# Performance work log

Hardware: AMD Instinct MI355X
Metric: run time of the kernel (lower is better)

Reference implementation:

```python
import jax, jax.numpy as jnp
import numpy as np

B, R, DIM = 4096, 64, 128


def setup_inputs() -> dict:
    key = jax.random.key(0)
    ks = jax.random.split(key, 8)
    return {
        "query_emb": jax.random.normal(ks[0], (B, DIM), jnp.float32),
        "offset_emb": jax.random.normal(ks[1], (B, DIM), jnp.float32),
        "refer_embs": jax.random.normal(ks[2], (B, R, DIM), jnp.float32),
        "query_r": jax.random.normal(ks[3], (B, DIM), jnp.float32),
        "refer_r": jax.random.normal(ks[4], (B, R, DIM), jnp.float32),
        "start_embs": jax.random.normal(ks[5], (B, R, DIM), jnp.float32),
        # attn_layer_1: Linear(2*dim, dim); xavier-uniform-like scale
        "W1": jax.random.uniform(ks[6], (DIM, 2 * DIM), jnp.float32, -0.125, 0.125),
        "b1": jnp.zeros((DIM,), jnp.float32),
        # attn_layer_2: Linear(dim, dim)
        "W2": jax.random.uniform(ks[7], (DIM, DIM), jnp.float32, -0.125, 0.125),
        "b2": jnp.zeros((DIM,), jnp.float32),
    }


def reference(query_emb, offset_emb, refer_embs, query_r, refer_r, start_embs, W1, b1, W2, b2):
    # bias term per neighbor: [B, R, dim]
    bias = refer_embs - (start_embs + refer_r)
    # concat([refer_r, broadcast(query_r)]) @ W1.T split to avoid materializing the concat:
    # W1 = [W1_a | W1_b] over the 2*dim input axis
    W1a, W1b = W1[:, :DIM], W1[:, DIM:]
    h = jnp.einsum('brd,kd->brk', refer_r, W1a) \
        + jnp.einsum('bd,kd->bk', query_r, W1b)[:, None, :] + b1
    h = jax.nn.relu(h)  # [B, R, dim]
    attn = jnp.einsum('brk,dk->brd', h, W2) + b2  # attn_layer_2
    final_refer_emb = jnp.sum(attn * bias, axis=-2)  # [B, dim]
    final_query_emb = query_emb + final_refer_emb
    return (final_query_emb, offset_emb)
```

## Files before the change

### kernel.cpp

```cpp
#include <hip/hip_runtime.h>
#include <hip/hip_bf16.h>
#include <stdint.h>

#define BTOT 4096
#define RR   64
#define DIMD 128
#define NB   8
#define NBLK (BTOT / NB)

typedef short s16x8 __attribute__((ext_vector_type(8)));
typedef float f32x4 __attribute__((ext_vector_type(4)));

__device__ __forceinline__ unsigned short f2bf(float x) {
  __hip_bfloat16 h = __float2bfloat16(x);
  return __builtin_bit_cast(unsigned short, h);
}
__device__ __forceinline__ float bf2f(unsigned short u) {
  unsigned int v = ((unsigned int)u) << 16;
  return __builtin_bit_cast(float, v);
}

__global__ __launch_bounds__(256) void prep_kernel(
    const float* __restrict__ W1, const float* __restrict__ b1,
    const float* __restrict__ query_r, const float* __restrict__ W2,
    float* __restrict__ qproj, unsigned short* __restrict__ w1a_swz,
    unsigned short* __restrict__ w2_swz)
{
  __shared__ float w1b[128 * 132];
  __shared__ float qrs[256];
  const int tid = threadIdx.x;

  {
    const int k = tid >> 1, d0 = (tid & 1) * 64;
    const float* src = W1 + k * 256 + 128 + d0;
    float* dst = &w1b[k * 132 + d0];
    #pragma unroll
    for (int i = 0; i < 64; i += 4)
      *reinterpret_cast<float4*>(dst + i) = *reinterpret_cast<const float4*>(src + i);
  }
  if (blockIdx.x < 2) {
    const float* Wsrc = (blockIdx.x == 0) ? W1 : W2;
    unsigned short* dstw = (blockIdx.x == 0) ? w1a_swz : w2_swz;
    const int stride = (blockIdx.x == 0) ? 256 : 128;
    for (int i = tid; i < 128 * 128; i += 256) {
      const int k = i >> 7, d = i & 127;
      dstw[k * 128 + (d ^ ((k & 7) << 3))] = f2bf(Wsrc[k * stride + d]);
    }
  }
  __syncthreads();

  const int b0 = blockIdx.x * NB;
  const int k = tid & 127, bh = tid >> 7;
  for (int p = 0; p < NB / 2; ++p) {
    const int b = b0 + p * 2;
    qrs[tid] = query_r[(size_t)(b + bh) * DIMD + k];
    __syncthreads();
    float acc = b1[k];
    const float* qq = &qrs[bh * 128];
    const float* wr = &w1b[k * 132];
    #pragma unroll
    for (int d = 0; d < 128; d += 4) {
      float4 wv = *reinterpret_cast<const float4*>(wr + d);
      float4 qv = *reinterpret_cast<const float4*>(qq + d);
      acc = fmaf(wv.x, qv.x, acc); acc = fmaf(wv.y, qv.y, acc);
      acc = fmaf(wv.z, qv.z, acc); acc = fmaf(wv.w, qv.w, acc);
    }
    qproj[(size_t)(b + bh) * DIMD + k] = acc;
    __syncthreads();
  }
}

__global__ __launch_bounds__(256, 2) void main_kernel(
    const float* __restrict__ query_emb, const float* __restrict__ offset_emb,
    const float* __restrict__ refer_embs, const float* __restrict__ refer_r,
    const float* __restrict__ start_embs, const float* __restrict__ b2,
    const float* __restrict__ qproj, const unsigned short* __restrict__ w1a_swz,
    const unsigned short* __restrict__ w2_swz, float* __restrict__ out)
{
  __shared__ unsigned short lds_w1a[128 * 128];
  __shared__ unsigned short lds_w2[128 * 128];
  __shared__ unsigned short lds_rr[4][16 * 128];

  const int tid  = threadIdx.x;
  const int wave = tid >> 6;
  const int lane = tid & 63;
  const int g    = lane >> 4;
  const int c    = lane & 15;

  {
    const uint4* s1 = reinterpret_cast<const uint4*>(w1a_swz);
    const uint4* s2 = reinterpret_cast<const uint4*>(w2_swz);
    uint4* d1 = reinterpret_cast<uint4*>(lds_w1a);
    uint4* d2 = reinterpret_cast<uint4*>(lds_w2);
    #pragma unroll
    for (int i = 0; i < 8; ++i) {
      d1[tid + 256 * i] = s1[tid + 256 * i];
      d2[tid + 256 * i] = s2[tid + 256 * i];
    }
  }
  __syncthreads();

  unsigned short* myrr = &lds_rr[wave][0];
  const int srl = lane >> 2;
  const int sd0 = (lane & 3) * 32;
  const int rl4 = 4 * g;

  for (int bb = 0; bb < NB; ++bb) {
    const int b = blockIdx.x * NB + bb;
    const size_t base = (size_t)b * RR * DIMD;

    const float* rp = refer_r + base + (size_t)(wave * 16 + srl) * DIMD + sd0;
    float4 fv[8];
    #pragma unroll
    for (int i = 0; i < 8; ++i) fv[i] = *reinterpret_cast<const float4*>(rp + 4 * i);

    const float* pre = refer_embs + base + (size_t)(wave * 16 + rl4) * DIMD + c;
    const float* pse = start_embs + base + (size_t)(wave * 16 + rl4) * DIMD + c;
    float rebv[32], sebv[32];
    #pragma unroll
    for (int nt = 0; nt < 8; ++nt)
      #pragma unroll
      for (int r = 0; r < 4; ++r) {
        rebv[nt * 4 + r] = pre[r * DIMD + nt * 16];
        sebv[nt * 4 + r] = pse[r * DIMD + nt * 16];
      }

    __syncthreads();

    {
      const int sw_s = (srl & 7) << 3;
      unsigned short* wrow = &myrr[srl * DIMD];
      #pragma unroll
      for (int gi = 0; gi < 4; ++gi) {
        union { unsigned short u[8]; uint4 v; } pk;
        const float4 a = fv[2 * gi], bq = fv[2 * gi + 1];
        pk.u[0] = f2bf(a.x);  pk.u[1] = f2bf(a.y);
        pk.u[2] = f2bf(a.z);  pk.u[3] = f2bf(a.w);
        pk.u[4] = f2bf(bq.x); pk.u[5] = f2bf(bq.y);
        pk.u[6] = f2bf(bq.z); pk.u[7] = f2bf(bq.w);
        *reinterpret_cast<uint4*>(&wrow[(sd0 + gi * 8) ^ sw_s]) = pk.v;
      }
    }
    asm volatile("s_waitcnt lgkmcnt(0)" ::: "memory");

    float rrv[32];
    #pragma unroll
    for (int nt = 0; nt < 8; ++nt)
      #pragma unroll
      for (int r = 0; r < 4; ++r) {
        const int rl = rl4 + r;
        const int d = nt * 16 + c;
        rrv[nt * 4 + r] = bf2f(myrr[rl * DIMD + (d ^ ((rl & 7) << 3))]);
      }
    s16x8 af[4];
    {
      const int sw = (c & 7) << 3;
      #pragma unroll
      for (int ks = 0; ks < 4; ++ks)
        af[ks] = *reinterpret_cast<const s16x8*>(&myrr[c * DIMD + ((ks * 32 + g * 8) ^ sw)]);
    }

    f32x4 Ch[8];
    #pragma unroll
    for (int nt = 0; nt < 8; ++nt) {
      const float qv = qproj[(size_t)b * DIMD + nt * 16 + c];
      Ch[nt] = (f32x4){qv, qv, qv, qv};
    }
    #pragma unroll
    for (int ks = 0; ks < 4; ++ks)
      #pragma unroll
      for (int nt = 0; nt < 8; ++nt) {
        const int kr = nt * 16 + c;
        s16x8 bf = *reinterpret_cast<const s16x8*>(
            &lds_w1a[kr * DIMD + ((ks * 32 + g * 8) ^ ((kr & 7) << 3))]);
        Ch[nt] = __builtin_amdgcn_mfma_f32_16x16x32_bf16(af[ks], bf, Ch[nt], 0, 0, 0);
      }

    float biasv[32];
    #pragma unroll
    for (int i = 0; i < 32; ++i) biasv[i] = rebv[i] - sebv[i] - rrv[i];

    asm volatile("s_waitcnt lgkmcnt(0)" ::: "memory");
    #pragma unroll
    for (int nt = 0; nt < 8; ++nt)
      #pragma unroll
      for (int r = 0; r < 4; ++r) {
        const int rl = rl4 + r;
        const int d = nt * 16 + c;
        myrr[rl * DIMD + (d ^ ((rl & 7) << 3))] = f2bf(fmaxf(Ch[nt][r], 0.f));
      }
    asm volatile("s_waitcnt lgkmcnt(0)" ::: "memory");

    s16x8 hf[4];
    {
      const int sw = (c & 7) << 3;
      #pragma unroll
      for (int ks = 0; ks < 4; ++ks)
        hf[ks] = *reinterpret_cast<const s16x8*>(&myrr[c * DIMD + ((ks * 32 + g * 8) ^ sw)]);
    }
    f32x4 Ca[8];
    #pragma unroll
    for (int nt = 0; nt < 8; ++nt) {
      const float bv = b2[nt * 16 + c];
      Ca[nt] = (f32x4){bv, bv, bv, bv};
    }
    #pragma unroll
    for (int ks = 0; ks < 4; ++ks)
      #pragma unroll
      for (int nt = 0; nt < 8; ++nt) {
        const int dr = nt * 16 + c;
        s16x8 wf = *reinterpret_cast<const s16x8*>(
            &lds_w2[dr * DIMD + ((ks * 32 + g * 8) ^ ((dr & 7) << 3))]);
        Ca[nt] = __builtin_amdgcn_mfma_f32_16x16x32_bf16(hf[ks], wf, Ca[nt], 0, 0, 0);
      }

    float psum[8];
    #pragma unroll
    for (int nt = 0; nt < 8; ++nt) {
      float s = 0.f;
      #pragma unroll
      for (int r = 0; r < 4; ++r) s = fmaf(Ca[nt][r], biasv[nt * 4 + r], s);
      s += __shfl_xor(s, 16);
      s += __shfl_xor(s, 32);
      psum[nt] = s;
    }
    float* pp = reinterpret_cast<float*>(&lds_rr[0][0]);
    __syncthreads();
    if (lane < 16) {
      #pragma unroll
      for (int nt = 0; nt < 8; ++nt) pp[wave * 128 + nt * 16 + c] = psum[nt];
    }
    __syncthreads();
    if (tid < 128) {
      const float s = pp[tid] + pp[tid + 128] + pp[tid + 256] + pp[tid + 384];
      out[(size_t)b * DIMD + tid] = query_emb[(size_t)b * DIMD + tid] + s;
    }
  }

  {
    const size_t ob = (size_t)blockIdx.x * NB * DIMD;
    #pragma unroll
    for (int i = 0; i < (NB * DIMD) / 256; ++i) {
      const size_t idx = ob + tid + 256 * i;
      out[(size_t)BTOT * DIMD + idx] = offset_emb[idx];
    }
  }
}

extern "C" void kernel_launch(void* const* d_in, const int* in_sizes, int n_in,
                              void* d_out, int out_size, void* d_ws, size_t ws_size,
                              hipStream_t stream) {
  const float* query_emb  = (const float*)d_in[0];
  const float* offset_emb = (const float*)d_in[1];
  const float* refer_embs = (const float*)d_in[2];
  const float* query_r    = (const float*)d_in[3];
  const float* refer_r    = (const float*)d_in[4];
  const float* start_embs = (const float*)d_in[5];
  const float* W1 = (const float*)d_in[6];
  const float* b1 = (const float*)d_in[7];
  const float* W2 = (const float*)d_in[8];
  const float* b2 = (const float*)d_in[9];
  float* out = (float*)d_out;

  float* qproj = (float*)d_ws;
  unsigned short* w1a_swz =
      (unsigned short*)((char*)d_ws + (size_t)BTOT * DIMD * sizeof(float));
  unsigned short* w2_swz = w1a_swz + 128 * 128;

  hipLaunchKernelGGL(prep_kernel, dim3(NBLK), dim3(256), 0, stream,
                     W1, b1, query_r, W2, qproj, w1a_swz, w2_swz);
  hipLaunchKernelGGL(main_kernel, dim3(NBLK), dim3(256), 0, stream,
                     query_emb, offset_emb, refer_embs, refer_r, start_embs,
                     b2, qproj, w1a_swz, w2_swz, out);
}
```

Baseline: 118.1 us.

## Assign whole batches per wave with register prefetch and vectorized bias loads

```diff
diff --git a/kernel.cpp b/kernel.cpp
--- a/kernel.cpp
+++ b/kernel.cpp
@@ -23,13 +23,19 @@
 __global__ __launch_bounds__(256) void prep_kernel(
     const float* __restrict__ W1, const float* __restrict__ b1,
     const float* __restrict__ query_r, const float* __restrict__ W2,
+    const float* __restrict__ offset_emb,
     float* __restrict__ qproj, unsigned short* __restrict__ w1a_swz,
-    unsigned short* __restrict__ w2_swz)
+    unsigned short* __restrict__ w2_swz, float* __restrict__ out)
 {
   __shared__ float w1b[128 * 132];
   __shared__ float qrs[256];
   const int tid = threadIdx.x;
 
+  {
+    const size_t ob = (size_t)blockIdx.x * NB * DIMD + (size_t)tid * 4;
+    *reinterpret_cast<float4*>(out + (size_t)BTOT * DIMD + ob) =
+        *reinterpret_cast<const float4*>(offset_emb + ob);
+  }
   {
     const int k = tid >> 1, d0 = (tid & 1) * 64;
     const float* src = W1 + k * 256 + 128 + d0;
@@ -71,7 +77,7 @@
 }
 
 __global__ __launch_bounds__(256, 2) void main_kernel(
-    const float* __restrict__ query_emb, const float* __restrict__ offset_emb,
+    const float* __restrict__ query_emb,
     const float* __restrict__ refer_embs, const float* __restrict__ refer_r,
     const float* __restrict__ start_embs, const float* __restrict__ b2,
     const float* __restrict__ qproj, const unsigned short* __restrict__ w1a_swz,
@@ -101,34 +107,44 @@
   __syncthreads();
 
   unsigned short* myrr = &lds_rr[wave][0];
-  const int srl = lane >> 2;
-  const int sd0 = (lane & 3) * 32;
-  const int rl4 = 4 * g;
-
-  for (int bb = 0; bb < NB; ++bb) {
-    const int b = blockIdx.x * NB + bb;
-    const size_t base = (size_t)b * RR * DIMD;
-
-    const float* rp = refer_r + base + (size_t)(wave * 16 + srl) * DIMD + sd0;
-    float4 fv[8];
-    #pragma unroll
-    for (int i = 0; i < 8; ++i) fv[i] = *reinterpret_cast<const float4*>(rp + 4 * i);
-
-    const float* pre = refer_embs + base + (size_t)(wave * 16 + rl4) * DIMD + c;
-    const float* pse = start_embs + base + (size_t)(wave * 16 + rl4) * DIMD + c;
-    float rebv[32], sebv[32];
-    #pragma unroll
-    for (int nt = 0; nt < 8; ++nt)
-      #pragma unroll
-      for (int r = 0; r < 4; ++r) {
-        rebv[nt * 4 + r] = pre[r * DIMD + nt * 16];
-        sebv[nt * 4 + r] = pse[r * DIMD + nt * 16];
-      }
-
-    __syncthreads();
+  const int srl  = lane >> 2;
+  const int sd0  = (lane & 3) * 32;
+  const int sw_s = (srl & 7) << 3;
+  const int swc  = (c & 7) << 3;
+  const int rl4  = 4 * g;
+
+  const int b0w = blockIdx.x * NB + wave * 2;
+
+  float b2v[8];
+  #pragma unroll
+  for (int nt = 0; nt < 8; ++nt) b2v[nt] = b2[nt * 16 + c];
+
+  float4 fv[8], ev[8], sv[8];
+  float qn[8], qe[8];
+  {
+    const size_t base = (size_t)b0w * RR * DIMD + (size_t)srl * DIMD + sd0;
+    #pragma unroll
+    for (int i = 0; i < 8; ++i) {
+      fv[i] = *reinterpret_cast<const float4*>(refer_r    + base + 4 * i);
+      ev[i] = *reinterpret_cast<const float4*>(refer_embs + base + 4 * i);
+      sv[i] = *reinterpret_cast<const float4*>(start_embs + base + 4 * i);
+    }
+    #pragma unroll
+    for (int nt = 0; nt < 8; ++nt) {
+      qn[nt] = qproj[(size_t)b0w * DIMD + nt * 16 + c];
+      qe[nt] = query_emb[(size_t)b0w * DIMD + nt * 16 + c];
+    }
+  }
+
+  float acc[8];
+  #pragma unroll
+  for (int nt = 0; nt < 8; ++nt) acc[nt] = 0.f;
+
+  #pragma unroll
+  for (int it = 0; it < 8; ++it) {
+    const int b = b0w + (it >> 2);
 
     {
-      const int sw_s = (srl & 7) << 3;
       unsigned short* wrow = &myrr[srl * DIMD];
       #pragma unroll
       for (int gi = 0; gi < 4; ++gi) {
@@ -141,108 +157,114 @@
         *reinterpret_cast<uint4*>(&wrow[(sd0 + gi * 8) ^ sw_s]) = pk.v;
       }
     }
-    asm volatile("s_waitcnt lgkmcnt(0)" ::: "memory");
-
-    float rrv[32];
+
+    uint4 bp[4];
+    #pragma unroll
+    for (int gi = 0; gi < 4; ++gi) {
+      union { unsigned short u[8]; uint4 v; } pk;
+      const float4 e0 = ev[2 * gi], s0 = sv[2 * gi], f0 = fv[2 * gi];
+      const float4 e1 = ev[2 * gi + 1], s1 = sv[2 * gi + 1], f1 = fv[2 * gi + 1];
+      pk.u[0] = f2bf(e0.x - s0.x - f0.x); pk.u[1] = f2bf(e0.y - s0.y - f0.y);
+      pk.u[2] = f2bf(e0.z - s0.z - f0.z); pk.u[3] = f2bf(e0.w - s0.w - f0.w);
+      pk.u[4] = f2bf(e1.x - s1.x - f1.x); pk.u[5] = f2bf(e1.y - s1.y - f1.y);
+      pk.u[6] = f2bf(e1.z - s1.z - f1.z); pk.u[7] = f2bf(e1.w - s1.w - f1.w);
+      bp[gi] = pk.v;
+    }
+
+    f32x4 Ch[8];
+    #pragma unroll
+    for (int nt = 0; nt < 8; ++nt) Ch[nt] = (f32x4){qn[nt], qn[nt], qn[nt], qn[nt]};
+
+    if (it + 1 < 8) {
+      const int bn = b0w + ((it + 1) >> 2);
+      const int rn = ((it + 1) & 3) * 16;
+      const size_t base = (size_t)bn * RR * DIMD + (size_t)(rn + srl) * DIMD + sd0;
+      #pragma unroll
+      for (int i = 0; i < 8; ++i) {
+        fv[i] = *reinterpret_cast<const float4*>(refer_r    + base + 4 * i);
+        ev[i] = *reinterpret_cast<const float4*>(refer_embs + base + 4 * i);
+        sv[i] = *reinterpret_cast<const float4*>(start_embs + base + 4 * i);
+      }
+    }
+
+    asm volatile("s_waitcnt lgkmcnt(0)" ::: "memory");
+
+    s16x8 af[4];
+    #pragma unroll
+    for (int ks = 0; ks < 4; ++ks)
+      af[ks] = *reinterpret_cast<const s16x8*>(&myrr[c * DIMD + ((ks * 32 + g * 8) ^ swc)]);
+    #pragma unroll
+    for (int ks = 0; ks < 4; ++ks)
+      #pragma unroll
+      for (int nt = 0; nt < 8; ++nt) {
+        s16x8 bf = *reinterpret_cast<const s16x8*>(
+            &lds_w1a[(nt * 16 + c) * DIMD + ((ks * 32 + g * 8) ^ swc)]);
+        Ch[nt] = __builtin_amdgcn_mfma_f32_16x16x32_bf16(af[ks], bf, Ch[nt], 0, 0, 0);
+      }
+
+    asm volatile("s_waitcnt lgkmcnt(0)" ::: "memory");
     #pragma unroll
     for (int nt = 0; nt < 8; ++nt)
       #pragma unroll
       for (int r = 0; r < 4; ++r) {
         const int rl = rl4 + r;
-        const int d = nt * 16 + c;
-        rrv[nt * 4 + r] = bf2f(myrr[rl * DIMD + (d ^ ((rl & 7) << 3))]);
-      }
-    s16x8 af[4];
+        myrr[rl * DIMD + ((nt * 16 + c) ^ ((rl & 7) << 3))] = f2bf(fmaxf(Ch[nt][r], 0.f));
+      }
+    asm volatile("s_waitcnt lgkmcnt(0)" ::: "memory");
+
+    s16x8 hf[4];
+    #pragma unroll
+    for (int ks = 0; ks < 4; ++ks)
+      hf[ks] = *reinterpret_cast<const s16x8*>(&myrr[c * DIMD + ((ks * 32 + g * 8) ^ swc)]);
+    f32x4 Ca[8];
+    #pragma unroll
+    for (int nt = 0; nt < 8; ++nt) Ca[nt] = (f32x4){b2v[nt], b2v[nt], b2v[nt], b2v[nt]};
+    #pragma unroll
+    for (int ks = 0; ks < 4; ++ks)
+      #pragma unroll
+      for (int nt = 0; nt < 8; ++nt) {
+        s16x8 wf = *reinterpret_cast<const s16x8*>(
+            &lds_w2[(nt * 16 + c) * DIMD + ((ks * 32 + g * 8) ^ swc)]);
+        Ca[nt] = __builtin_amdgcn_mfma_f32_16x16x32_bf16(hf[ks], wf, Ca[nt], 0, 0, 0);
+      }
+
     {
-      const int sw = (c & 7) << 3;
-      #pragma unroll
-      for (int ks = 0; ks < 4; ++ks)
-        af[ks] = *reinterpret_cast<const s16x8*>(&myrr[c * DIMD + ((ks * 32 + g * 8) ^ sw)]);
-    }
-
-    f32x4 Ch[8];
+      unsigned short* wrow = &myrr[srl * DIMD];
+      #pragma unroll
+      for (int gi = 0; gi < 4; ++gi)
+        *reinterpret_cast<uint4*>(&wrow[(sd0 + gi * 8) ^ sw_s]) = bp[gi];
+    }
+    asm volatile("s_waitcnt lgkmcnt(0)" ::: "memory");
+
     #pragma unroll
     for (int nt = 0; nt < 8; ++nt) {
-      const float qv = qproj[(size_t)b * DIMD + nt * 16 + c];
-      Ch[nt] = (f32x4){qv, qv, qv, qv};
-    }
-    #pragma unroll
-    for (int ks = 0; ks < 4; ++ks)
-      #pragma unroll
-      for (int nt = 0; nt < 8; ++nt) {
-        const int kr = nt * 16 + c;
-        s16x8 bf = *reinterpret_cast<const s16x8*>(
-            &lds_w1a[kr * DIMD + ((ks * 32 + g * 8) ^ ((kr & 7) << 3))]);
-        Ch[nt] = __builtin_amdgcn_mfma_f32_16x16x32_bf16(af[ks], bf, Ch[nt], 0, 0, 0);
-      }
-
-    float biasv[32];
-    #pragma unroll
-    for (int i = 0; i < 32; ++i) biasv[i] = rebv[i] - sebv[i] - rrv[i];
-
-    asm volatile("s_waitcnt lgkmcnt(0)" ::: "memory");
-    #pragma unroll
-    for (int nt = 0; nt < 8; ++nt)
+      float s = 0.f;
       #pragma unroll
       for (int r = 0; r < 4; ++r) {
         const int rl = rl4 + r;
-        const int d = nt * 16 + c;
-        myrr[rl * DIMD + (d ^ ((rl & 7) << 3))] = f2bf(fmaxf(Ch[nt][r], 0.f));
-      }
-    asm volatile("s_waitcnt lgkmcnt(0)" ::: "memory");
-
-    s16x8 hf[4];
-    {
-      const int sw = (c & 7) << 3;
-      #pragma unroll
-      for (int ks = 0; ks < 4; ++ks)
-        hf[ks] = *reinterpret_cast<const s16x8*>(&myrr[c * DIMD + ((ks * 32 + g * 8) ^ sw)]);
-    }
-    f32x4 Ca[8];
-    #pragma unroll
-    for (int nt = 0; nt < 8; ++nt) {
-      const float bv = b2[nt * 16 + c];
-      Ca[nt] = (f32x4){bv, bv, bv, bv};
-    }
-    #pragma unroll
-    for (int ks = 0; ks < 4; ++ks)
-      #pragma unroll
-      for (int nt = 0; nt < 8; ++nt) {
-        const int dr = nt * 16 + c;
-        s16x8 wf = *reinterpret_cast<const s16x8*>(
-            &lds_w2[dr * DIMD + ((ks * 32 + g * 8) ^ ((dr & 7) << 3))]);
-        Ca[nt] = __builtin_amdgcn_mfma_f32_16x16x32_bf16(hf[ks], wf, Ca[nt], 0, 0, 0);
-      }
-
-    float psum[8];
-    #pragma unroll
-    for (int nt = 0; nt < 8; ++nt) {
-      float s = 0.f;
-      #pragma unroll
-      for (int r = 0; r < 4; ++r) s = fmaf(Ca[nt][r], biasv[nt * 4 + r], s);
+        const float bcv = bf2f(myrr[rl * DIMD + ((nt * 16 + c) ^ ((rl & 7) << 3))]);
+        s = fmaf(Ca[nt][r], bcv, s);
+      }
       s += __shfl_xor(s, 16);
       s += __shfl_xor(s, 32);
-      psum[nt] = s;
-    }
-    float* pp = reinterpret_cast<float*>(&lds_rr[0][0]);
-    __syncthreads();
-    if (lane < 16) {
-      #pragma unroll
-      for (int nt = 0; nt < 8; ++nt) pp[wave * 128 + nt * 16 + c] = psum[nt];
-    }
-    __syncthreads();
-    if (tid < 128) {
-      const float s = pp[tid] + pp[tid + 128] + pp[tid + 256] + pp[tid + 384];
-      out[(size_t)b * DIMD + tid] = query_emb[(size_t)b * DIMD + tid] + s;
-    }
-  }
-
-  {
-    const size_t ob = (size_t)blockIdx.x * NB * DIMD;
-    #pragma unroll
-    for (int i = 0; i < (NB * DIMD) / 256; ++i) {
-      const size_t idx = ob + tid + 256 * i;
-      out[(size_t)BTOT * DIMD + idx] = offset_emb[idx];
+      acc[nt] += s;
+    }
+
+    if ((it & 3) == 3) {
+      if (lane < 16) {
+        #pragma unroll
+        for (int nt = 0; nt < 8; ++nt)
+          out[(size_t)b * DIMD + nt * 16 + c] = qe[nt] + acc[nt];
+      }
+      #pragma unroll
+      for (int nt = 0; nt < 8; ++nt) acc[nt] = 0.f;
+      if (it < 7) {
+        #pragma unroll
+        for (int nt = 0; nt < 8; ++nt) {
+          qn[nt] = qproj[(size_t)(b + 1) * DIMD + nt * 16 + c];
+          qe[nt] = query_emb[(size_t)(b + 1) * DIMD + nt * 16 + c];
+        }
+      }
     }
   }
 }
@@ -268,8 +290,8 @@
   unsigned short* w2_swz = w1a_swz + 128 * 128;
 
   hipLaunchKernelGGL(prep_kernel, dim3(NBLK), dim3(256), 0, stream,
-                     W1, b1, query_r, W2, qproj, w1a_swz, w2_swz);
+                     W1, b1, query_r, W2, offset_emb, qproj, w1a_swz, w2_swz, out);
   hipLaunchKernelGGL(main_kernel, dim3(NBLK), dim3(256), 0, stream,
-                     query_emb, offset_emb, refer_embs, refer_r, start_embs,
+                     query_emb, refer_embs, refer_r, start_embs,
                      b2, qproj, w1a_swz, w2_swz, out);
 }
```

Result: slower. 188.1 us (+59.3%).
